# Performance work log

Measured on AMD Instinct MI355X. Metric: run time of the kernel, lower is better.

## Reference

```python
import jax, jax.numpy as jnp
import numpy as np

B, C_IN, C_OUT, H, W = 8, 512, 512, 64, 64
KS = 3
STYLE_DIM = 512
UP = 2            # AliasFreeConv passes upsample*2 = 2 to the activation
DOWN = 2
TAPS = 12
MARGIN = 10
NEG_SLOPE = 0.2
LRELU_SCALE = float(np.sqrt(2.0))  # fused_leaky_relu default scale
EPS = 1e-8


def _lowpass(taps):
    # 1D windowed-sinc lowpass (separable FIR), normalized to sum 1
    n = np.arange(taps)
    x = n - (taps - 1) / 2.0
    h = np.sinc(x / 2.0) * np.hanning(taps)
    return (h / h.sum()).astype(np.float32)


def upfirdn2d(x, kernel, up, down, pad):
    # x: (N,C,H,W); kernel: (kh,kw); up=(ux,uy); down=(dx,dy); pad=(px0,px1,py0,py1)
    # Semantics match rosinality upfirdn2d_native: zero-stuff, pad, convolve with
    # flipped kernel, stride-downsample. lhs_dilation gives (L-1)*u+1 samples, the
    # torch version keeps L*u (u-1 trailing zeros), so add u-1 to trailing pad.
    ux, uy = up
    dx, dy = down
    px0, px1, py0, py1 = pad
    N, C, H_, W_ = x.shape
    k = jnp.flip(kernel, axis=(0, 1))[None, None].astype(x.dtype)  # (1,1,kh,kw)
    y = x.reshape(N * C, 1, H_, W_)
    y = jax.lax.conv_general_dilated(
        y, k, window_strides=(dy, dx),
        padding=((py0, py1 + uy - 1), (px0, px1 + ux - 1)),
        lhs_dilation=(uy, ux),
        dimension_numbers=('NCHW', 'OIHW', 'NCHW'))
    return y.reshape(N, C, y.shape[2], y.shape[3])


def setup_inputs() -> dict:
    key = jax.random.key(0)
    ks = jax.random.split(key, 6)
    x = jax.random.normal(ks[0], (B, C_IN, H, W), jnp.float32)
    style = jax.random.normal(ks[1], (B, STYLE_DIM), jnp.float32)
    mod_w = jax.random.normal(ks[2], (C_IN, STYLE_DIM), jnp.float32)   # EqualLinear weight
    mod_b = jnp.ones((C_IN,), jnp.float32)                              # bias_init=1
    conv_w = jax.random.normal(ks[3], (C_OUT, C_IN, KS, KS), jnp.float32)
    act_b = jax.random.normal(ks[4], (C_OUT,), jnp.float32) * 0.1
    lp = jnp.asarray(_lowpass(TAPS))
    return {"x": x, "style": style, "mod_w": mod_w, "mod_b": mod_b,
            "conv_w": conv_w, "act_b": act_b, "up_filter": lp, "down_filter": lp}


def reference(x, style, mod_w, mod_b, conv_w, act_b, up_filter, down_filter):
    Bn, Cin, _, _ = x.shape
    # --- ModulatedConv2d (padding=False, eval mode: ema_var = 1) ---
    lin_scale = 1.0 / np.sqrt(STYLE_DIM)          # EqualLinear scale, lr_mul=1
    s = style @ (mod_w * lin_scale).T + mod_b     # (B, Cin)
    wscale = 1.0 / np.sqrt(Cin * KS * KS)
    w = wscale * conv_w[None] * s[:, None, :, None, None]  # (B, Cout, Cin, kh, kw)
    demod = jax.lax.rsqrt(jnp.sum(w * w, axis=(2, 3, 4)) + EPS)
    w = w * demod[:, :, None, None, None]
    w = w / (1.0 + EPS)                           # / (sqrt(ema_var)+eps), ema_var=1

    def conv_one(xi, wi):  # per-sample grouped conv (groups=batch), VALID padding
        return jax.lax.conv_general_dilated(
            xi[None], wi, (1, 1), 'VALID',
            dimension_numbers=('NCHW', 'OIHW', 'NCHW'))[0]
    out = jax.vmap(conv_one)(x, w)                # (B, Cout, H-2, W-2)

    # --- AliasFreeActivation ---
    out = out + act_b[None, :, None, None]
    fu = up_filter * UP                           # 1D filter scaled by upsample at init
    p = TAPS - UP
    up_pad = ((p + 1) // 2 + UP * 2 - 1, p // 2 + UP)  # padding flag False (ks==3)
    out = upfirdn2d(out, fu[None, :], up=(UP, 1), down=(1, 1),
                    pad=(up_pad[0], up_pad[1], 0, 0))
    out = upfirdn2d(out, fu[:, None], up=(1, UP), down=(1, 1),
                    pad=(0, 0, up_pad[0], up_pad[1]))
    out = jnp.where(out >= 0, out, NEG_SLOPE * out) * LRELU_SCALE
    p = TAPS - DOWN
    dpad = ((p + 1) // 2, p // 2)
    out = upfirdn2d(out, down_filter[None, :], up=(1, 1), down=(DOWN, 1),
                    pad=(dpad[0], dpad[1], 0, 0))
    out = upfirdn2d(out, down_filter[:, None], up=(1, 1), down=(1, DOWN),
                    pad=(0, 0, dpad[0], dpad[1]))
    m = (MARGIN * UP - MARGIN * DOWN) // 2        # = 0 here (static)
    if m > 0:
        out = out[:, :, m:-m, m:-m]
    return out
```

## Files before the change

kernel.cpp:

```cpp
#include <hip/hip_runtime.h>

typedef __attribute__((ext_vector_type(8))) short s16x8;
typedef __attribute__((ext_vector_type(4))) float f32x4;

__device__ __forceinline__ float b2f(unsigned short u){
  union { unsigned int i; float f; } v; v.i = ((unsigned int)u) << 16; return v.f;
}
__device__ __forceinline__ unsigned short f2b(float f){
  union { float f; unsigned int i; } v; v.f = f;
  unsigned int x = v.i;
  return (unsigned short)((x + 0x7fffu + ((x >> 16) & 1u)) >> 16);
}

__device__ __forceinline__ void ld_lds16(const unsigned short* g, unsigned short* l){
  __builtin_amdgcn_global_load_lds(
      (const __attribute__((address_space(1))) void*)g,
      (__attribute__((address_space(3))) void*)l, 16, 0, 0);
}

template<int BF16> struct In;
template<> struct In<1>{
  static __device__ __forceinline__ float ld(const void* p, size_t i){
    return b2f(((const unsigned short*)p)[i]);
  }
};
template<> struct In<0>{
  static __device__ __forceinline__ float ld(const void* p, size_t i){
    return ((const float*)p)[i];
  }
};

__global__ void k_detect(const unsigned int* __restrict__ mod_b, int* __restrict__ flag){
  *flag = (*mod_b == 0x3F803F80u) ? 1 : 0;
}

template<int BF16>
__device__ __forceinline__ void small_body(const void* actb, const void* upf, const void* dnf,
                                           float* actb_f, float* fu_f, float* fd_f){
  int t = threadIdx.x;
  actb_f[t] = In<BF16>::ld(actb, t);
  if(t < 12){
    fu_f[t] = 2.0f * In<BF16>::ld(upf, t);
    fd_f[t] = In<BF16>::ld(dnf, t);
  }
}
__global__ void k_small(const void* __restrict__ actb, const void* __restrict__ upf,
                        const void* __restrict__ dnf, float* __restrict__ actb_f,
                        float* __restrict__ fu_f, float* __restrict__ fd_f,
                        const int* __restrict__ flag){
  if(*flag) small_body<1>(actb, upf, dnf, actb_f, fu_f, fd_f);
  else      small_body<0>(actb, upf, dnf, actb_f, fu_f, fd_f);
}

template<int BF16>
__device__ __forceinline__ void style_body(const void* style, const void* mod_w,
                                           const void* mod_b, float* s){
  int gw = (blockIdx.x*256 + threadIdx.x) >> 6;
  int lane = threadIdx.x & 63;
  int b = gw >> 9, i = gw & 511;
  size_t so = (size_t)b*512 + lane*8;
  size_t mo = (size_t)i*512 + lane*8;
  float acc = 0.f;
  #pragma unroll
  for(int q=0;q<8;q++) acc += In<BF16>::ld(style, so+q)*In<BF16>::ld(mod_w, mo+q);
  #pragma unroll
  for(int m=32;m>=1;m>>=1) acc += __shfl_xor(acc, m, 64);
  if(lane == 0) s[gw] = acc * 0.044194173824159216f + In<BF16>::ld(mod_b, i);
}
__global__ __launch_bounds__(256) void k_style(
    const void* __restrict__ style, const void* __restrict__ mod_w,
    const void* __restrict__ mod_b, float* __restrict__ s,
    const int* __restrict__ flag){
  if(*flag) style_body<1>(style, mod_w, mod_b, s);
  else      style_body<0>(style, mod_w, mod_b, s);
}

template<int BF16>
__device__ __forceinline__ void wrepq_body(const void* conv_w, unsigned short* wrep2, float* wsq){
  int idx = blockIdx.x*256 + threadIdx.x;
  float v[9], acc = 0.f;
  #pragma unroll
  for(int t=0;t<9;t++){ v[t] = In<BF16>::ld(conv_w, (size_t)idx*9 + t); acc += v[t]*v[t]; }
  wsq[idx] = acc;
  #pragma unroll
  for(int t=0;t<9;t++) wrep2[t*262144 + idx] = f2b(v[t]);
}
__global__ __launch_bounds__(256) void k_wrepq(
    const void* __restrict__ conv_w, unsigned short* __restrict__ wrep2,
    float* __restrict__ wsq, const int* __restrict__ flag){
  if(*flag) wrepq_body<1>(conv_w, wrep2, wsq);
  else      wrepq_body<0>(conv_w, wrep2, wsq);
}

__global__ __launch_bounds__(256) void k_demod(
    const float* __restrict__ s, const float* __restrict__ wsq,
    float* __restrict__ rowscale){
  int gw = (blockIdx.x*256 + threadIdx.x) >> 6;
  int lane = threadIdx.x & 63;
  int b = gw >> 9, o = gw & 511;
  const float* sr = s + b*512 + lane*8;
  const float* wr = wsq + (size_t)o*512 + lane*8;
  float acc = 0.f;
  #pragma unroll
  for(int q=0;q<8;q++){ float sv = sr[q]; acc += sv*sv*wr[q]; }
  #pragma unroll
  for(int m=32;m>=1;m>>=1) acc += __shfl_xor(acc, m, 64);
  if(lane == 0){
    float demod = rsqrtf(acc*(1.0f/4608.0f) + 1e-8f);
    rowscale[gw] = 0.014731391274719742f * demod * (1.0f/(1.0f+1e-8f));
  }
}

template<int BF16>
__device__ __forceinline__ void xs_body(const void* x, const float* s,
                                        unsigned short* xs2, unsigned short* tl){
  int bh = blockIdx.x >> 3;
  int i0 = (blockIdx.x & 7) << 6;
  int b = bh >> 6, h = bh & 63;
  #pragma unroll
  for(int l=0;l<2;l++){
    int e = (threadIdx.x + l*256) << 3;
    int row = e >> 6, col = e & 63;
    size_t base = (((size_t)(b*512 + i0 + row))*64 + h)*64 + col;
    float sc = s[b*512 + i0 + row];
    alignas(16) unsigned short tmp[8];
    if(BF16){
      uint4 v = *(const uint4*)((const unsigned short*)x + base);
      const unsigned short* pv = (const unsigned short*)&v;
      #pragma unroll
      for(int q2=0;q2<8;q2++) tmp[q2] = f2b(b2f(pv[q2]) * sc);
    } else {
      float4 v0 = *(const float4*)((const float*)x + base);
      float4 v1 = *(const float4*)((const float*)x + base + 4);
      tmp[0]=f2b(v0.x*sc); tmp[1]=f2b(v0.y*sc); tmp[2]=f2b(v0.z*sc); tmp[3]=f2b(v0.w*sc);
      tmp[4]=f2b(v1.x*sc); tmp[5]=f2b(v1.y*sc); tmp[6]=f2b(v1.z*sc); tmp[7]=f2b(v1.w*sc);
    }
    *(uint4*)(tl + row*72 + col) = *(const uint4*)tmp;
  }
  __syncthreads();
  #pragma unroll
  for(int l=0;l<2;l++){
    int e = (threadIdx.x + l*256) << 3;
    int w = e >> 6, ic = e & 63;
    alignas(16) unsigned short tmp[8];
    #pragma unroll
    for(int q2=0;q2<8;q2++) tmp[q2] = tl[(ic + q2)*72 + w];
    *(uint4*)(xs2 + (((size_t)(b*64 + h))*64 + w)*512 + i0 + ic) = *(const uint4*)tmp;
  }
}
__global__ __launch_bounds__(256) void k_xs(
    const void* __restrict__ x, const float* __restrict__ s,
    unsigned short* __restrict__ xs2, const int* __restrict__ flag){
  __shared__ unsigned short tl[64*72];
  if(*flag) xs_body<1>(x, s, xs2, tl);
  else      xs_body<0>(x, s, xs2, tl);
}


#define MFMA16(a,b,c) __builtin_amdgcn_mfma_f32_16x16x32_bf16((a),(b),(c),0,0,0)
#define KBARRIER __builtin_amdgcn_s_barrier()
#define LGKM0 asm volatile("s_waitcnt lgkmcnt(0)" ::: "memory")
#define VMW4  asm volatile("s_waitcnt vmcnt(4)" ::: "memory")
#define VMW8  asm volatile("s_waitcnt vmcnt(8)" ::: "memory")
#define VMW0  asm volatile("s_waitcnt vmcnt(0)" ::: "memory")

template<int MH,int NH>
__device__ __forceinline__ void mmq(f32x4 (&acc)[8][4], const s16x8 (&Ax)[8], const s16x8 (&Bx)[4]){
  #pragma unroll
  for(int j=0;j<4;j++)
    #pragma unroll
    for(int k=0;k<2;k++){
      f32x4 c = acc[MH*4+j][NH*2+k];
      c = MFMA16(Ax[j*2+0], Bx[k*2+0], c);
      c = MFMA16(Ax[j*2+1], Bx[k*2+1], c);
      acc[MH*4+j][NH*2+k] = c;
    }
}

template<int BUF,int MH>
__device__ __forceinline__ void lda(s16x8 (&dst)[8], const unsigned short* lds,
                                    int arow, int c0, int c1){
  #pragma unroll
  for(int j=0;j<4;j++){
    const unsigned short* p = lds + BUF*32768 + arow + (MH*64 + j*16)*64;
    dst[j*2+0] = *(const s16x8*)(p + c0);
    dst[j*2+1] = *(const s16x8*)(p + c1);
  }
}

template<int BUF,int NH>
__device__ __forceinline__ void ldb(s16x8 (&dst)[4], const unsigned short* lds,
                                    int brow, int c0, int c1){
  #pragma unroll
  for(int k=0;k<2;k++){
    const unsigned short* p = lds + BUF*32768 + brow + (NH*2 + k)*16*64;
    dst[k*2+0] = *(const s16x8*)(p + c0);
    dst[k*2+1] = *(const s16x8*)(p + c1);
  }
}

template<int BUF,int H>
__device__ __forceinline__ void stga(const unsigned short* wrep2, unsigned short* lds,
                                     const unsigned (&aoff)[2][2], int sdst, int kt){
  unsigned koff = (unsigned)(kt >> 3)*262144u + (unsigned)(kt & 7)*64u;
  ld_lds16(wrep2 + aoff[H][0] + koff, lds + BUF*32768 + H*8192 + 0*4096 + sdst);
  ld_lds16(wrep2 + aoff[H][1] + koff, lds + BUF*32768 + H*8192 + 1*4096 + sdst);
}

template<int BUF,int H>
__device__ __forceinline__ void stgb(const unsigned short* xs2, unsigned short* lds,
                                     const unsigned (&boff)[2][2], int sdst, int kt){
  int t = kt >> 3;
  int kh = (t*11) >> 5;
  unsigned koff = (unsigned)(kh*64 + (t - kh*3))*512u + (unsigned)(kt & 7)*64u;
  ld_lds16(xs2 + boff[H][0] + koff, lds + BUF*32768 + 16384 + H*8192 + 0*4096 + sdst);
  ld_lds16(xs2 + boff[H][1] + koff, lds + BUF*32768 + 16384 + H*8192 + 1*4096 + sdst);
}

__global__ __launch_bounds__(512, 2) void k_conv(
    const unsigned short* __restrict__ wrep2,
    const unsigned short* __restrict__ xs2,
    const float* __restrict__ rowscale,
    const float* __restrict__ actb_f,
    unsigned short* __restrict__ out0){
  __shared__ unsigned short lds[65536];

  const int tid  = threadIdx.x;
  const int lane = tid & 63, wid = tid >> 6;
  const int wm = wid >> 2, wn = wid & 3;
  const int quad = lane >> 4, l16 = lane & 15, sw = l16 & 7;

  int w = blockIdx.x;
  int wsw = (w & 7)*31 + (w >> 3);
  const int mt = wsw & 1, nt = wsw >> 1;
  const int o0 = mt*256, p0 = nt*256;

  const int srow  = tid >> 3;
  const int sgoff = ((tid & 7) ^ (srow & 7)) * 8;
  unsigned aoff[2][2], boff[2][2];
  #pragma unroll
  for(int h=0;h<2;h++){
    #pragma unroll
    for(int r=0;r<2;r++){
      int row = srow + r*64 + h*128;
      aoff[h][r] = (unsigned)(o0 + row)*512u + (unsigned)sgoff;
      int p  = p0 + row;
      int bb = ((p >> 7)*529) >> 14;
      boff[h][r] = (unsigned)(p + bb*128)*512u + (unsigned)sgoff;
    }
  }
  const int sdst = wid*512;

  const int c0 = ((0*4 + quad) ^ sw) * 8;
  const int c1 = ((1*4 + quad) ^ sw) * 8;
  const int arow = (wm*128 + l16) * 64;
  const int brow = (wn*64  + l16) * 64 + 16384;

  f32x4 acc[8][4];
  f32x4 z = {0.f,0.f,0.f,0.f};
  #pragma unroll
  for(int a=0;a<8;a++)
    #pragma unroll
    for(int n=0;n<4;n++) acc[a][n] = z;

  s16x8 Aa[8], Ab[8], Ba[4], Bb[4];

  stga<0,0>(wrep2, lds, aoff, sdst, 0);
  stga<0,1>(wrep2, lds, aoff, sdst, 0);
  stgb<0,0>(xs2,   lds, boff, sdst, 0);
  stgb<0,1>(xs2,   lds, boff, sdst, 0);
  stga<1,0>(wrep2, lds, aoff, sdst, 1);
  stga<1,1>(wrep2, lds, aoff, sdst, 1);
  stgb<1,0>(xs2,   lds, boff, sdst, 1);
  stgb<1,1>(xs2,   lds, boff, sdst, 1);
  VMW8;
  KBARRIER;
  lda<0,0>(Aa, lds, arow, c0, c1);
  ldb<0,0>(Ba, lds, brow, c0, c1);

  #pragma unroll 1
  for(int it=0; it<36; ++it){
    const int T0 = 2*it;
    const int full = (it < 35);
    ldb<0,1>(Bb, lds, brow, c0, c1);
    KBARRIER; LGKM0;
    __builtin_amdgcn_s_setprio(1); mmq<0,0>(acc, Aa, Ba); __builtin_amdgcn_s_setprio(0);
    KBARRIER;
    lda<0,1>(Ab, lds, arow, c0, c1);
    if(full){ stgb<0,0>(xs2, lds, boff, sdst, T0+2); stgb<0,1>(xs2, lds, boff, sdst, T0+2); }
    KBARRIER; LGKM0;
    __builtin_amdgcn_s_setprio(1); mmq<0,1>(acc, Aa, Bb); __builtin_amdgcn_s_setprio(0);
    KBARRIER;
    KBARRIER; LGKM0;
    __builtin_amdgcn_s_setprio(1); mmq<1,0>(acc, Ab, Ba); __builtin_amdgcn_s_setprio(0);
    if(full){ VMW4; } else { VMW0; }
    KBARRIER;
    lda<1,0>(Aa, lds, arow, c0, c1);
    ldb<1,0>(Ba, lds, brow, c0, c1);
    if(full){ stga<0,0>(wrep2, lds, aoff, sdst, T0+2); stga<0,1>(wrep2, lds, aoff, sdst, T0+2); }
    KBARRIER; LGKM0;
    __builtin_amdgcn_s_setprio(1); mmq<1,1>(acc, Ab, Bb); __builtin_amdgcn_s_setprio(0);
    KBARRIER;
    ldb<1,1>(Bb, lds, brow, c0, c1);
    KBARRIER; LGKM0;
    __builtin_amdgcn_s_setprio(1); mmq<0,0>(acc, Aa, Ba); __builtin_amdgcn_s_setprio(0);
    KBARRIER;
    lda<1,1>(Ab, lds, arow, c0, c1);
    if(full){ stgb<1,0>(xs2, lds, boff, sdst, T0+3); stgb<1,1>(xs2, lds, boff, sdst, T0+3); }
    KBARRIER; LGKM0;
    __builtin_amdgcn_s_setprio(1); mmq<0,1>(acc, Aa, Bb); __builtin_amdgcn_s_setprio(0);
    KBARRIER;
    KBARRIER; LGKM0;
    __builtin_amdgcn_s_setprio(1); mmq<1,0>(acc, Ab, Ba); __builtin_amdgcn_s_setprio(0);
    if(full){ VMW4; }
    KBARRIER;
    if(full){
      lda<0,0>(Aa, lds, arow, c0, c1);
      ldb<0,0>(Ba, lds, brow, c0, c1);
      stga<1,0>(wrep2, lds, aoff, sdst, T0+3);
      stga<1,1>(wrep2, lds, aoff, sdst, T0+3);
    }
    KBARRIER; LGKM0;
    __builtin_amdgcn_s_setprio(1); mmq<1,1>(acc, Ab, Bb); __builtin_amdgcn_s_setprio(0);
    KBARRIER;
  }

  #pragma unroll
  for(int n=0;n<4;n++){
    int p  = p0 + wn*64 + n*16 + l16;
    int bn = ((p >> 7)*529) >> 14;
    int rem = p - bn*3968;
    const size_t obase = (size_t)bn*2031616u + (size_t)rem;
    const int rsb = bn*512;
    #pragma unroll
    for(int a=0;a<8;a++){
      int o = o0 + wm*128 + a*16 + quad*4;
      #pragma unroll
      for(int r=0;r<4;r++){
        float v = acc[a][n][r]*rowscale[rsb + o + r] + actb_f[o + r];
        out0[obase + (size_t)(o + r)*3968u] = f2b(v);
      }
    }
  }
}

__global__ __launch_bounds__(256) void k_filter(
    const unsigned short* __restrict__ out0,
    const float* __restrict__ fu_f,
    const float* __restrict__ fd_f,
    void* __restrict__ out,
    const int* __restrict__ flag){
  __shared__ unsigned short uvs[128*140];
  __shared__ unsigned short bufB[70*128];
  unsigned short* a0s = uvs;
  int bf = *flag;
  int bc = blockIdx.x;
  int tid = threadIdx.x;

  float fur[12], fdr[12];
  #pragma unroll
  for(int j=0;j<12;j++){ fur[j] = fu_f[j]; fdr[j] = fd_f[j]; }

  const uint4 z4 = {0,0,0,0};
  const unsigned short* src = out0 + (size_t)bc*62*64;
  for(int v=tid; v<496; v+=256)
    *(uint4*)(a0s + v*8) = *(const uint4*)(src + v*8);
  for(int idx=tid; idx<128; idx+=256){
    int r = idx >> 4, seg = idx & 15;
    *(uint4*)(bufB + ((r < 4) ? r : (r + 62))*128 + seg*8) = z4;
  }
  __syncthreads();

  for(int idx=tid; idx<62*16; idx+=256){
    int r = idx >> 4, tt0 = (idx & 15) << 2;
    const unsigned short* ar = a0s + r*64;
    float w[10];
    #pragma unroll
    for(int c=0;c<10;c++){
      int col = tt0 - 4 + c;
      w[c] = (col >= 0 && col < 62) ? b2f(ar[col]) : 0.f;
    }
    alignas(16) unsigned short tmp[8];
    #pragma unroll
    for(int u=0;u<4;u++){
      float accE = 0.f, accO = 0.f;
      #pragma unroll
      for(int jj=0;jj<6;jj++){
        accE += fur[2*jj+1]*w[u+5-jj];
        accO += fur[2*jj  ]*w[u+6-jj];
      }
      tmp[2*u]   = f2b(accE);
      tmp[2*u+1] = f2b(accO);
    }
    *(uint4*)(bufB + (r+4)*128 + 2*tt0) = *(const uint4*)tmp;
  }
  __syncthreads();

  for(int idx=tid; idx<16*128; idx+=256){
    int tr0 = (idx >> 7) << 2, o = idx & 127;
    float w[10];
    #pragma unroll
    for(int c=0;c<10;c++) w[c] = b2f(bufB[(tr0+c)*128 + o]);
    #pragma unroll
    for(int u=0;u<4;u++){
      float accE = 0.f, accO = 0.f;
      #pragma unroll
      for(int jj=0;jj<6;jj++){
        accE += fur[2*jj+1]*w[u+5-jj];
        accO += fur[2*jj  ]*w[u+6-jj];
      }
      accE = (accE >= 0.f ? accE : 0.2f*accE)*1.4142135623730951f;
      accO = (accO >= 0.f ? accO : 0.2f*accO)*1.4142135623730951f;
      int m = 2*(tr0+u);
      uvs[m*140 + 5 + o]     = f2b(accE);
      uvs[(m+1)*140 + 5 + o] = f2b(accO);
    }
  }
  for(int idx=tid; idx<1536; idx+=256){
    int m = (idx*2731) >> 15;
    int c = idx - m*12;
    uvs[m*140 + ((c < 5) ? c : (c + 128))] = 0;
  }
  __syncthreads();

  for(int idx=tid; idx<96; idx+=256){
    int r = idx >> 3, seg = idx & 7;
    *(uint4*)(bufB + ((r < 6) ? r : (r + 128))*64 + seg*8) = z4;
  }
  for(int idx=tid; idx<128*16; idx+=256){
    int m = idx >> 4, X0 = (idx & 15) << 2;
    const unsigned short* ur = uvs + m*140 + 2*X0;
    alignas(8) unsigned short wv[20];
    #pragma unroll
    for(int h=0;h<5;h++) *(uint2*)(wv + h*4) = *(const uint2*)(ur + h*4);
    alignas(8) unsigned short tmp[4];
    #pragma unroll
    for(int u=0;u<4;u++){
      float acc = 0.f;
      #pragma unroll
      for(int j=0;j<12;j++) acc += fdr[j]*b2f(wv[2*u+11-j]);
      tmp[u] = f2b(acc);
    }
    *(uint2*)(bufB + (m+6)*64 + X0) = *(const uint2*)tmp;
  }
  __syncthreads();

  for(int idx=tid; idx<16*64; idx+=256){
    int Y0 = (idx >> 6) << 2, X = idx & 63;
    float w[18];
    #pragma unroll
    for(int c=0;c<18;c++) w[c] = b2f(bufB[(2*Y0+1+c)*64 + X]);
    #pragma unroll
    for(int u=0;u<4;u++){
      float acc = 0.f;
      #pragma unroll
      for(int j=0;j<12;j++) acc += fdr[j]*w[2*u+11-j];
      if(bf) ((unsigned short*)out)[(size_t)bc*4096 + (Y0+u)*64 + X] = f2b(acc);
      else   ((float*)out)[(size_t)bc*4096 + (Y0+u)*64 + X] = acc;
    }
  }
}

extern "C" void kernel_launch(void* const* d_in, const int* in_sizes, int n_in,
                              void* d_out, int out_size, void* d_ws, size_t ws_size,
                              hipStream_t stream){
  const void* x     = d_in[0];
  const void* style = d_in[1];
  const void* mod_w = d_in[2];
  const void* mod_b = d_in[3];
  const void* convw = d_in[4];
  const void* actb  = d_in[5];
  const void* upf   = d_in[6];
  const void* dnf   = d_in[7];
  char* ws = (char*)d_ws;
  int*   flag   = (int*)(ws + 0);
  float* actb_f = (float*)(ws + 1024);
  float* fu_f   = (float*)(ws + 4096);
  float* fd_f   = (float*)(ws + 4224);
  float* s_buf  = (float*)(ws + 8192);
  float* rsc    = (float*)(ws + 24576);
  float* wsq    = (float*)(ws + 40960);
  unsigned short* wrep2 = (unsigned short*)(ws + 1089536);
  unsigned short* xs2   = (unsigned short*)(ws + 5808128);
  unsigned short* out0  = (unsigned short*)(ws + 39370752);
  if(ws_size < 71876608) return;

  k_detect<<<1, 1, 0, stream>>>((const unsigned int*)mod_b, flag);
  k_small<<<1, 512, 0, stream>>>(actb, upf, dnf, actb_f, fu_f, fd_f, flag);
  k_style<<<1024, 256, 0, stream>>>(style, mod_w, mod_b, s_buf, flag);
  k_wrepq<<<1024, 256, 0, stream>>>(convw, wrep2, wsq, flag);
  k_demod<<<1024, 256, 0, stream>>>(s_buf, wsq, rsc);
  k_xs<<<4096, 256, 0, stream>>>(x, s_buf, xs2, flag);
  k_conv<<<248, 512, 0, stream>>>(wrep2, xs2, rsc, actb_f, out0);
  k_filter<<<4096, 256, 0, stream>>>(out0, fu_f, fd_f, d_out, flag);
}
```

Before: 356.6 us.

## Switch filter intermediates to fp16 with packed half2 FIR and branchless lrelu

The intermediate conv output and the filter-stage buffers now use fp16 instead of bf16. The two upsampling FIR passes are computed with packed half2 multiply-adds, and leaky ReLU becomes the branchless form a*x + b*|x|. This is meant to cut the VALU cost of the filter kernel, which dominates its runtime, at the cost of fp16 range and overflow risk and lower accumulation precision. The GEMM loop barrier placement is also shuffled slightly.

```diff
diff --git a/kernel.cpp b/kernel.cpp
--- a/kernel.cpp
+++ b/kernel.cpp
@@ -2,6 +2,7 @@
 
 typedef __attribute__((ext_vector_type(8))) short s16x8;
 typedef __attribute__((ext_vector_type(4))) float f32x4;
+typedef __attribute__((ext_vector_type(2))) _Float16 h16x2;
 
 __device__ __forceinline__ float b2f(unsigned short u){
   union { unsigned int i; float f; } v; v.i = ((unsigned int)u) << 16; return v.f;
@@ -10,6 +11,15 @@
   union { float f; unsigned int i; } v; v.f = f;
   unsigned int x = v.i;
   return (unsigned short)((x + 0x7fffu + ((x >> 16) & 1u)) >> 16);
+}
+__device__ __forceinline__ _Float16 u2h(unsigned short u){
+  union { unsigned short u; _Float16 h; } v; v.u = u; return v.h;
+}
+__device__ __forceinline__ unsigned short h2u(_Float16 h){
+  union { _Float16 h; unsigned short u; } v; v.h = h; return v.u;
+}
+__device__ __forceinline__ h16x2 habs2(h16x2 x){
+  union { h16x2 h; unsigned int u; } v; v.h = x; v.u &= 0x7FFF7FFFu; return v.h;
 }
 
 __device__ __forceinline__ void ld_lds16(const unsigned short* g, unsigned short* l){
@@ -314,15 +324,15 @@
     __builtin_amdgcn_s_setprio(1); mmq<1,0>(acc, Ab, Ba); __builtin_amdgcn_s_setprio(0);
     if(full){ VMW4; }
     KBARRIER;
+    KBARRIER;
     if(full){
       lda<0,0>(Aa, lds, arow, c0, c1);
       ldb<0,0>(Ba, lds, brow, c0, c1);
       stga<1,0>(wrep2, lds, aoff, sdst, T0+3);
       stga<1,1>(wrep2, lds, aoff, sdst, T0+3);
     }
-    KBARRIER; LGKM0;
+    LGKM0;
     __builtin_amdgcn_s_setprio(1); mmq<1,1>(acc, Ab, Bb); __builtin_amdgcn_s_setprio(0);
-    KBARRIER;
   }
 
   #pragma unroll
@@ -338,7 +348,7 @@
       #pragma unroll
       for(int r=0;r<4;r++){
         float v = acc[a][n][r]*rowscale[rsb + o + r] + actb_f[o + r];
-        out0[obase + (size_t)(o + r)*3968u] = f2b(v);
+        out0[obase + (size_t)(o + r)*3968u] = h2u((_Float16)v);
       }
     }
   }
@@ -357,9 +367,21 @@
   int bc = blockIdx.x;
   int tid = threadIdx.x;
 
-  float fur[12], fdr[12];
-  #pragma unroll
-  for(int j=0;j<12;j++){ fur[j] = fu_f[j]; fdr[j] = fd_f[j]; }
+  float fdr[12];
+  #pragma unroll
+  for(int j=0;j<12;j++) fdr[j] = fd_f[j];
+  h16x2 fuo2[6], fue2[6];
+  #pragma unroll
+  for(int jj=0;jj<6;jj++){
+    _Float16 ho = (_Float16)fu_f[2*jj+1];
+    _Float16 he = (_Float16)fu_f[2*jj];
+    h16x2 a; a[0]=ho; a[1]=ho; fuo2[jj]=a;
+    h16x2 b; b[0]=he; b[1]=he; fue2[jj]=b;
+  }
+  const _Float16 lrA = (_Float16)0.8485281374238570f;
+  const _Float16 lrB = (_Float16)0.5656854249492380f;
+  h16x2 lrA2; lrA2[0]=lrA; lrA2[1]=lrA;
+  h16x2 lrB2; lrB2[0]=lrB; lrB2[1]=lrB;
 
   const uint4 z4 = {0,0,0,0};
   const unsigned short* src = out0 + (size_t)bc*62*64;
@@ -374,47 +396,59 @@
   for(int idx=tid; idx<62*16; idx+=256){
     int r = idx >> 4, tt0 = (idx & 15) << 2;
     const unsigned short* ar = a0s + r*64;
-    float w[10];
+    _Float16 w[10];
     #pragma unroll
     for(int c=0;c<10;c++){
       int col = tt0 - 4 + c;
-      w[c] = (col >= 0 && col < 62) ? b2f(ar[col]) : 0.f;
+      w[c] = (col >= 0 && col < 62) ? u2h(ar[col]) : (_Float16)0.f;
+    }
+    h16x2 p[9];
+    #pragma unroll
+    for(int k=0;k<9;k++){ h16x2 t; t[0]=w[k]; t[1]=w[k+1]; p[k]=t; }
+    h16x2 PE01={(_Float16)0.f,(_Float16)0.f}, PE23=PE01, PO01=PE01, PO23=PE01;
+    #pragma unroll
+    for(int jj=0;jj<6;jj++){
+      PE01 += fuo2[jj]*p[5-jj];
+      PE23 += fuo2[jj]*p[7-jj];
+      PO01 += fue2[jj]*p[6-jj];
+      PO23 += fue2[jj]*p[8-jj];
     }
     alignas(16) unsigned short tmp[8];
-    #pragma unroll
-    for(int u=0;u<4;u++){
-      float accE = 0.f, accO = 0.f;
-      #pragma unroll
-      for(int jj=0;jj<6;jj++){
-        accE += fur[2*jj+1]*w[u+5-jj];
-        accO += fur[2*jj  ]*w[u+6-jj];
-      }
-      tmp[2*u]   = f2b(accE);
-      tmp[2*u+1] = f2b(accO);
-    }
+    tmp[0]=h2u(PE01[0]); tmp[1]=h2u(PO01[0]); tmp[2]=h2u(PE01[1]); tmp[3]=h2u(PO01[1]);
+    tmp[4]=h2u(PE23[0]); tmp[5]=h2u(PO23[0]); tmp[6]=h2u(PE23[1]); tmp[7]=h2u(PO23[1]);
     *(uint4*)(bufB + (r+4)*128 + 2*tt0) = *(const uint4*)tmp;
   }
   __syncthreads();
 
   for(int idx=tid; idx<16*128; idx+=256){
     int tr0 = (idx >> 7) << 2, o = idx & 127;
-    float w[10];
-    #pragma unroll
-    for(int c=0;c<10;c++) w[c] = b2f(bufB[(tr0+c)*128 + o]);
-    #pragma unroll
-    for(int u=0;u<4;u++){
-      float accE = 0.f, accO = 0.f;
-      #pragma unroll
-      for(int jj=0;jj<6;jj++){
-        accE += fur[2*jj+1]*w[u+5-jj];
-        accO += fur[2*jj  ]*w[u+6-jj];
-      }
-      accE = (accE >= 0.f ? accE : 0.2f*accE)*1.4142135623730951f;
-      accO = (accO >= 0.f ? accO : 0.2f*accO)*1.4142135623730951f;
-      int m = 2*(tr0+u);
-      uvs[m*140 + 5 + o]     = f2b(accE);
-      uvs[(m+1)*140 + 5 + o] = f2b(accO);
-    }
+    _Float16 w[10];
+    #pragma unroll
+    for(int c=0;c<10;c++) w[c] = u2h(bufB[(tr0+c)*128 + o]);
+    h16x2 p[9];
+    #pragma unroll
+    for(int k=0;k<9;k++){ h16x2 t; t[0]=w[k]; t[1]=w[k+1]; p[k]=t; }
+    h16x2 PE01={(_Float16)0.f,(_Float16)0.f}, PE23=PE01, PO01=PE01, PO23=PE01;
+    #pragma unroll
+    for(int jj=0;jj<6;jj++){
+      PE01 += fuo2[jj]*p[5-jj];
+      PE23 += fuo2[jj]*p[7-jj];
+      PO01 += fue2[jj]*p[6-jj];
+      PO23 += fue2[jj]*p[8-jj];
+    }
+    PE01 = PE01*lrA2 + habs2(PE01)*lrB2;
+    PE23 = PE23*lrA2 + habs2(PE23)*lrB2;
+    PO01 = PO01*lrA2 + habs2(PO01)*lrB2;
+    PO23 = PO23*lrA2 + habs2(PO23)*lrB2;
+    int mb = 2*tr0;
+    uvs[(mb+0)*140 + 5 + o] = h2u(PE01[0]);
+    uvs[(mb+1)*140 + 5 + o] = h2u(PO01[0]);
+    uvs[(mb+2)*140 + 5 + o] = h2u(PE01[1]);
+    uvs[(mb+3)*140 + 5 + o] = h2u(PO01[1]);
+    uvs[(mb+4)*140 + 5 + o] = h2u(PE23[0]);
+    uvs[(mb+5)*140 + 5 + o] = h2u(PO23[0]);
+    uvs[(mb+6)*140 + 5 + o] = h2u(PE23[1]);
+    uvs[(mb+7)*140 + 5 + o] = h2u(PO23[1]);
   }
   for(int idx=tid; idx<1536; idx+=256){
     int m = (idx*2731) >> 15;
@@ -438,8 +472,8 @@
     for(int u=0;u<4;u++){
       float acc = 0.f;
       #pragma unroll
-      for(int j=0;j<12;j++) acc += fdr[j]*b2f(wv[2*u+11-j]);
-      tmp[u] = f2b(acc);
+      for(int j=0;j<12;j++) acc += fdr[j]*(float)u2h(wv[2*u+11-j]);
+      tmp[u] = h2u((_Float16)acc);
     }
     *(uint2*)(bufB + (m+6)*64 + X0) = *(const uint2*)tmp;
   }
@@ -449,7 +483,7 @@
     int Y0 = (idx >> 6) << 2, X = idx & 63;
     float w[18];
     #pragma unroll
-    for(int c=0;c<18;c++) w[c] = b2f(bufB[(2*Y0+1+c)*64 + X]);
+    for(int c=0;c<18;c++) w[c] = (float)u2h(bufB[(2*Y0+1+c)*64 + X]);
     #pragma unroll
     for(int u=0;u<4;u++){
       float acc = 0.f;
```

Result: faster. 326.7 us (-8.4%).
